# Kernel optimization log

Hardware: AMD Instinct MI355X
Metric: run time of the kernel (lower is better)

The kernel has to match this reference:

```python
import jax, jax.numpy as jnp
import numpy as np

B, N, D, H, C = 2048, 6, 2048, 1024, 200  # batch, nodes/graph, feat dim, hidden, classes
ALPHA = 0.015   # distance decay in edge weight
SCALE = 24.0    # weight rescale after mean-subtraction + clamp


def setup_inputs() -> dict:
    key = jax.random.key(0)
    k1, k2, k3, k4 = jax.random.split(key, 4)
    part_feats = jax.random.normal(k1, (B, N, D), dtype=jnp.float32)
    # cdds columns: [score, y0, x0, y1, x1, idx]; only cols 1:5 (box coords) are used
    cdds = jax.random.uniform(k2, (B, N, 6), dtype=jnp.float32) * 448.0
    fc_w = jax.random.normal(k3, (2 * D, H), dtype=jnp.float32) * 0.02
    fc_b = jnp.zeros((H,), dtype=jnp.float32)
    cls_w = jax.random.normal(k4, (H, C), dtype=jnp.float32) * 0.02
    cls_b = jnp.zeros((C,), dtype=jnp.float32)
    return {"part_feats": part_feats, "cdds": cdds, "fc_w": fc_w, "fc_b": fc_b,
            "cls_w": cls_w, "cls_b": cls_b}


def reference(part_feats, cdds, fc_w, fc_b, cls_w, cls_b):
    # --- edge weights on per-sample complete graph (apply_edges) ---
    loc = cdds[:, :, 1:5]                      # (B, N, 4) = (y0, x0, y1, x1)
    cy = (loc[..., 0] + loc[..., 2]) * 0.5     # node center y, (B, N)
    cx = (loc[..., 1] + loc[..., 3]) * 0.5     # node center x, (B, N)
    dx = cx[:, :, None] - cx[:, None, :]       # (B, N, N) pairwise
    dy = cy[:, :, None] - cy[:, None, :]
    d2 = dx * dx + dy * dy
    mask = ~jnp.eye(N, dtype=bool)             # off-diagonal = real edges (30 per graph)
    dist = jnp.sqrt(jnp.where(mask, d2, 1.0))  # safe sqrt off the diagonal
    w0 = jnp.where(mask, jnp.exp(-ALPHA * dist), 0.0)
    mean_w = jnp.sum(w0, axis=(1, 2), keepdims=True) / (N * (N - 1))  # mean over 30 edges
    w = SCALE * jnp.maximum(w0 - mean_w, 0.0) * mask                  # (B, N, N), w[b,u,v]
    # --- update_all: u_mul_e + mean over the (N-1) incoming edges per node ---
    hidden = jnp.einsum('buv,bud->bvd', w, part_feats) / (N - 1)      # (B, N, D)
    # --- node MLP + graph mean readout + classifier ---
    node_ft = jnp.concatenate([hidden, part_feats], axis=-1) @ fc_w + fc_b  # (B, N, H)
    g_ft = node_ft.mean(axis=1)                                             # (B, H)
    return g_ft @ cls_w + cls_b                                             # (B, C)
```

## Files before the change

kernel.cpp:

```cpp
#include <hip/hip_runtime.h>
#include <math.h>

namespace {
constexpr int NB = 2048;
constexpr int NNODE = 6;
constexpr int DD = 2048;
constexpr int HH = 1024;
constexpr int CC = 200;
constexpr int K2 = 2 * DD;
constexpr int NPAD = 256;
constexpr int ZF = 8;
constexpr float ALPHA_C = 0.015f;
constexpr float SCALE_C = 24.0f;
}

typedef __attribute__((ext_vector_type(8))) short bf16x8;
typedef __attribute__((ext_vector_type(4))) float f32x4;

static __device__ __forceinline__ unsigned short f2bf(float x) {
    union { float f; unsigned int u; } v; v.f = x;
    unsigned int r = v.u + 0x7FFFu + ((v.u >> 16) & 1u);
    return (unsigned short)(r >> 16);
}

static __device__ __forceinline__ float bf2f(unsigned short u) {
    union { unsigned int i; float f; } v; v.i = ((unsigned int)u) << 16;
    return v.f;
}

static __device__ __forceinline__ float compute_s_lane(const float* __restrict__ cdds,
                                                       int b, int* u_out) {
    const int lane = threadIdx.x & 63;
    const int u = lane >> 3;
    const int v = lane & 7;
    *u_out = u;
    const float* cd = cdds + (size_t)b * 36;
    float w = 0.f;
    const bool valid = (u < 6) & (v < 6) & (u != v);
    if (u < 6 && v < 6 && u != v) {
        float cyu = (cd[u * 6 + 1] + cd[u * 6 + 3]) * 0.5f;
        float cxu = (cd[u * 6 + 2] + cd[u * 6 + 4]) * 0.5f;
        float cyv = (cd[v * 6 + 1] + cd[v * 6 + 3]) * 0.5f;
        float cxv = (cd[v * 6 + 2] + cd[v * 6 + 4]) * 0.5f;
        float dx = cxu - cxv, dy = cyu - cyv;
        w = expf(-ALPHA_C * sqrtf(dx * dx + dy * dy));
    }
    float s = w;
#pragma unroll
    for (int m = 32; m >= 1; m >>= 1) s += __shfl_xor(s, m);
    float mean = s * (1.f / 30.f);
    float tt = valid ? fmaxf(w - mean, 0.f) : 0.f;
    tt += __shfl_xor(tt, 1);
    tt += __shfl_xor(tt, 2);
    tt += __shfl_xor(tt, 4);
    return SCALE_C * tt * 0.2f;
}

__global__ __launch_bounds__(256) void k_small(const float* __restrict__ cls_w,
                                               const float* __restrict__ fc_b,
                                               const float* __restrict__ cls_b,
                                               const float* __restrict__ cdds,
                                               float* __restrict__ bvec,
                                               float* __restrict__ sbuf)
{
    __shared__ float red[256];
    const int bx = blockIdx.x;
    const int t = threadIdx.x;
    if (bx >= 25) {
        const int b = (bx - 25) * 4 + (t >> 6);
        int u;
        float su = compute_s_lane(cdds, b, &u);
        if ((t & 7) == 0 && u < 6) sbuf[b * 6 + u] = su;
        return;
    }
    int c8 = t & 7;
    int hs = t >> 3;
    int c = bx * 8 + c8;
    float acc = 0.f;
    for (int h = hs; h < HH; h += 32)
        acc += fc_b[h] * cls_w[(size_t)h * CC + c];
    red[t] = acc;
    __syncthreads();
    for (int s = 128; s >= 8; s >>= 1) {
        if (t < s) red[t] += red[t + s];
        __syncthreads();
    }
    if (t < 8) bvec[c] = red[t] + cls_b[c];
}

__global__ __launch_bounds__(256) void k_g1(const float* __restrict__ fc_w,
                                            const float* __restrict__ cls_w,
                                            unsigned short* __restrict__ Mt)
{
    __shared__ short As[32][68];
    __shared__ short Bs[64][68];
    const int t = threadIdx.x;
    const int lane = t & 63;
    const int wid = t >> 6;
    const int wm = wid >> 1, wn = wid & 1;
    const int bm = blockIdx.x * 32;
    const int bn = blockIdx.y * 64;

    f32x4 acc[2] = {};

    for (int k0 = 0; k0 < HH; k0 += 64) {
#pragma unroll
        for (int c = 0; c < 2; ++c) {
            int i = t + c * 256;
            int row = i >> 4;
            int k4 = (i & 15) << 2;
            float4 v = *(const float4*)(fc_w + (size_t)(bm + row) * HH + k0 + k4);
            ushort4 o;
            o.x = f2bf(v.x); o.y = f2bf(v.y); o.z = f2bf(v.z); o.w = f2bf(v.w);
            *(ushort4*)&As[row][k4] = o;
        }
#pragma unroll
        for (int c = 0; c < 4; ++c) {
            int i = t + c * 256;
            int kr = i >> 4;
            int n4 = (i & 15) << 2;
            const float* sp = cls_w + (size_t)(k0 + kr) * CC + bn + n4;
            float4 v = {0.f, 0.f, 0.f, 0.f};
            if (bn + n4 + 3 < CC) {
                v = *(const float4*)sp;
            } else {
                if (bn + n4 + 0 < CC) v.x = sp[0];
                if (bn + n4 + 1 < CC) v.y = sp[1];
                if (bn + n4 + 2 < CC) v.z = sp[2];
                if (bn + n4 + 3 < CC) v.w = sp[3];
            }
            Bs[n4 + 0][kr] = (short)f2bf(v.x);
            Bs[n4 + 1][kr] = (short)f2bf(v.y);
            Bs[n4 + 2][kr] = (short)f2bf(v.z);
            Bs[n4 + 3][kr] = (short)f2bf(v.w);
        }
        __syncthreads();
#pragma unroll
        for (int ks = 0; ks < 2; ++ks) {
            int kk = ks * 32 + ((lane >> 4) << 3);
            int ar = lane & 15;
            bf16x8 a = *(const bf16x8*)&As[wm * 16 + ar][kk];
#pragma unroll
            for (int fn = 0; fn < 2; ++fn) {
                bf16x8 b = *(const bf16x8*)&Bs[wn * 32 + fn * 16 + ar][kk];
                acc[fn] = __builtin_amdgcn_mfma_f32_16x16x32_bf16(a, b, acc[fn], 0, 0, 0);
            }
        }
        __syncthreads();
    }
#pragma unroll
    for (int fn = 0; fn < 2; ++fn) {
        int gm0 = bm + wm * 16 + ((lane >> 4) << 2);
        int gn = bn + wn * 32 + fn * 16 + (lane & 15);
        ushort4 o;
        o.x = f2bf(acc[fn][0]); o.y = f2bf(acc[fn][1]);
        o.z = f2bf(acc[fn][2]); o.w = f2bf(acc[fn][3]);
        *(ushort4*)(Mt + (size_t)gn * K2 + gm0) = o;
    }
}

__global__ __launch_bounds__(256) void k_fused(const float* __restrict__ pf,
                                               const float* __restrict__ sbuf,
                                               const unsigned short* __restrict__ Mt,
                                               unsigned short* __restrict__ part)
{
    __shared__ short Ap[32][36], Aq[32][36];
    __shared__ short Bp[256][36], Bq[256][36];
    const int t = threadIdx.x;
    const int lane = t & 63;
    const int wid = t >> 6;
    const int bm = blockIdx.x * 32;
    const int z = blockIdx.y;
    const int kbase = z * (DD / ZF);

    const int r = t >> 3;
    const int k4 = (t & 7) << 2;
    const float* sb = sbuf + (size_t)(bm + r) * 6;
    const float s0 = sb[0], s1 = sb[1], s2 = sb[2];
    const float s3 = sb[3], s4 = sb[4], s5 = sb[5];
    const float* pfb = pf + (size_t)(bm + r) * NNODE * DD + kbase + k4;

    f32x4 acc[2][4] = {};

    for (int ks = 0; ks < (DD / ZF) / 32; ++ks) {
        const int k0 = ks * 32;
        float4 v0 = *(const float4*)(pfb + k0 + 0 * DD);
        float4 v1 = *(const float4*)(pfb + k0 + 1 * DD);
        float4 v2 = *(const float4*)(pfb + k0 + 2 * DD);
        float4 v3 = *(const float4*)(pfb + k0 + 3 * DD);
        float4 v4 = *(const float4*)(pfb + k0 + 4 * DD);
        float4 v5 = *(const float4*)(pfb + k0 + 5 * DD);
#pragma unroll
        for (int c = 0; c < 4; ++c) {
            int i = t + c * 256;
            int n = i >> 2;
            int k8 = (i & 3) << 3;
            *(uint4*)&Bp[n][k8] =
                *(const uint4*)(Mt + (size_t)n * K2 + kbase + k0 + k8);
            *(uint4*)&Bq[n][k8] =
                *(const uint4*)(Mt + (size_t)n * K2 + DD + kbase + k0 + k8);
        }
        float4 q;
        q.x = v0.x + v1.x + v2.x + v3.x + v4.x + v5.x;
        q.y = v0.y + v1.y + v2.y + v3.y + v4.y + v5.y;
        q.z = v0.z + v1.z + v2.z + v3.z + v4.z + v5.z;
        q.w = v0.w + v1.w + v2.w + v3.w + v4.w + v5.w;
        float4 p = {0.f, 0.f, 0.f, 0.f};
        p.x = fmaf(s0, v0.x, p.x); p.y = fmaf(s0, v0.y, p.y);
        p.z = fmaf(s0, v0.z, p.z); p.w = fmaf(s0, v0.w, p.w);
        p.x = fmaf(s1, v1.x, p.x); p.y = fmaf(s1, v1.y, p.y);
        p.z = fmaf(s1, v1.z, p.z); p.w = fmaf(s1, v1.w, p.w);
        p.x = fmaf(s2, v2.x, p.x); p.y = fmaf(s2, v2.y, p.y);
        p.z = fmaf(s2, v2.z, p.z); p.w = fmaf(s2, v2.w, p.w);
        p.x = fmaf(s3, v3.x, p.x); p.y = fmaf(s3, v3.y, p.y);
        p.z = fmaf(s3, v3.z, p.z); p.w = fmaf(s3, v3.w, p.w);
        p.x = fmaf(s4, v4.x, p.x); p.y = fmaf(s4, v4.y, p.y);
        p.z = fmaf(s4, v4.z, p.z); p.w = fmaf(s4, v4.w, p.w);
        p.x = fmaf(s5, v5.x, p.x); p.y = fmaf(s5, v5.y, p.y);
        p.z = fmaf(s5, v5.z, p.z); p.w = fmaf(s5, v5.w, p.w);
        ushort4 pb, qb;
        pb.x = f2bf(p.x); pb.y = f2bf(p.y); pb.z = f2bf(p.z); pb.w = f2bf(p.w);
        qb.x = f2bf(q.x); qb.y = f2bf(q.y); qb.z = f2bf(q.z); qb.w = f2bf(q.w);
        *(ushort4*)&Ap[r][k4] = pb;
        *(ushort4*)&Aq[r][k4] = qb;
        __syncthreads();
        {
            int kk = (lane >> 4) << 3;
            int ar = lane & 15;
            bf16x8 ap0 = *(const bf16x8*)&Ap[ar][kk];
            bf16x8 ap1 = *(const bf16x8*)&Ap[16 + ar][kk];
            bf16x8 aq0 = *(const bf16x8*)&Aq[ar][kk];
            bf16x8 aq1 = *(const bf16x8*)&Aq[16 + ar][kk];
#pragma unroll
            for (int fn = 0; fn < 4; ++fn) {
                bf16x8 bp = *(const bf16x8*)&Bp[wid * 64 + fn * 16 + ar][kk];
                bf16x8 bq = *(const bf16x8*)&Bq[wid * 64 + fn * 16 + ar][kk];
                acc[0][fn] = __builtin_amdgcn_mfma_f32_16x16x32_bf16(ap0, bp, acc[0][fn], 0, 0, 0);
                acc[1][fn] = __builtin_amdgcn_mfma_f32_16x16x32_bf16(ap1, bp, acc[1][fn], 0, 0, 0);
                acc[0][fn] = __builtin_amdgcn_mfma_f32_16x16x32_bf16(aq0, bq, acc[0][fn], 0, 0, 0);
                acc[1][fn] = __builtin_amdgcn_mfma_f32_16x16x32_bf16(aq1, bq, acc[1][fn], 0, 0, 0);
            }
        }
        __syncthreads();
    }
#pragma unroll
    for (int fm = 0; fm < 2; ++fm)
#pragma unroll
        for (int fn = 0; fn < 4; ++fn) {
            int gm0 = bm + fm * 16 + ((lane >> 4) << 2);
            int gn = wid * 64 + fn * 16 + (lane & 15);
#pragma unroll
            for (int rr = 0; rr < 4; ++rr)
                part[((size_t)z * NB + gm0 + rr) * NPAD + gn] = f2bf(acc[fm][fn][rr]);
        }
}

__global__ __launch_bounds__(256) void k_combine(const unsigned short* __restrict__ part,
                                                 const float* __restrict__ bvec,
                                                 float* __restrict__ out)
{
    int idx = blockIdx.x * blockDim.x + threadIdx.x;
    if (idx >= NB * (CC / 4)) return;
    int b = idx / (CC / 4);
    int c0 = (idx - b * (CC / 4)) << 2;
    float s0 = 0.f, s1 = 0.f, s2 = 0.f, s3 = 0.f;
#pragma unroll
    for (int z = 0; z < ZF; ++z) {
        ushort4 v = *(const ushort4*)(part + ((size_t)z * NB + b) * NPAD + c0);
        s0 += bf2f(v.x); s1 += bf2f(v.y); s2 += bf2f(v.z); s3 += bf2f(v.w);
    }
    float4 o;
    o.x = s0 * (1.f / 6.f) + bvec[c0 + 0];
    o.y = s1 * (1.f / 6.f) + bvec[c0 + 1];
    o.z = s2 * (1.f / 6.f) + bvec[c0 + 2];
    o.w = s3 * (1.f / 6.f) + bvec[c0 + 3];
    *(float4*)(out + (size_t)b * CC + c0) = o;
}

extern "C" void kernel_launch(void* const* d_in, const int* in_sizes, int n_in,
                              void* d_out, int out_size, void* d_ws, size_t ws_size,
                              hipStream_t stream)
{
    const float* part_feats = (const float*)d_in[0];
    const float* cdds = (const float*)d_in[1];
    const float* fc_w = (const float*)d_in[2];
    const float* fc_b = (const float*)d_in[3];
    const float* cls_w = (const float*)d_in[4];
    const float* cls_b = (const float*)d_in[5];
    float* out = (float*)d_out;

    char* ws = (char*)d_ws;
    size_t off = 0;
    unsigned short* Mt = (unsigned short*)(ws + off);   off += (size_t)NPAD * K2 * 2;
    unsigned short* part = (unsigned short*)(ws + off); off += (size_t)ZF * NB * NPAD * 2;
    float* bvec = (float*)(ws + off);                   off += 256 * 4;
    float* sbuf = (float*)(ws + off);                   off += (size_t)NB * NNODE * 4;

    k_small<<<dim3(25 + NB / 4), dim3(256), 0, stream>>>(
        cls_w, fc_b, cls_b, cdds, bvec, sbuf);
    k_g1<<<dim3(K2 / 32, NPAD / 64), dim3(256), 0, stream>>>(fc_w, cls_w, Mt);
    k_fused<<<dim3(NB / 32, ZF), dim3(256), 0, stream>>>(part_feats, sbuf, Mt, part);
    k_combine<<<dim3((NB * (CC / 4) + 255) / 256), dim3(256), 0, stream>>>(part, bvec, out);
}
```

Measured before the change: 86.23 us.

## Split node reduction into a bf16 pq buffer and run a plain split-K GEMM

The weighted and plain node reductions (p and q) move out of the GEMM kernel. They now run in extra blocks of the Mt-building kernel, which write a bf16 [B, 2D] activation buffer. The second GEMM becomes a standard bf16 GEMM with 64-row tiles, 64-deep K steps and 16-way split-K, reading that buffer. This lets the streaming pass over part_feats overlap with the small weight GEMM and gives the main GEMM more reuse per tile. In exchange it adds a round trip of the bf16 buffer through global memory and doubles the partial-sum traffic in the combine step.

```diff
diff --git a/kernel.cpp b/kernel.cpp
--- a/kernel.cpp
+++ b/kernel.cpp
@@ -9,9 +9,12 @@
 constexpr int CC = 200;
 constexpr int K2 = 2 * DD;
 constexpr int NPAD = 256;
-constexpr int ZF = 8;
+constexpr int ZS2 = 16;
 constexpr float ALPHA_C = 0.015f;
 constexpr float SCALE_C = 24.0f;
+
+constexpr int G1_BLOCKS = 512;
+constexpr int PQ_UNITS = NB * 2;
 }
 
 typedef __attribute__((ext_vector_type(8))) short bf16x8;
@@ -88,18 +91,70 @@
     if (t < 8) bvec[c] = red[t] + cls_b[c];
 }
 
-__global__ __launch_bounds__(256) void k_g1(const float* __restrict__ fc_w,
-                                            const float* __restrict__ cls_w,
-                                            unsigned short* __restrict__ Mt)
+__global__ __launch_bounds__(256) void k_mid(const float* __restrict__ pf,
+                                             const float* __restrict__ sbuf,
+                                             const float* __restrict__ fc_w,
+                                             const float* __restrict__ cls_w,
+                                             unsigned short* __restrict__ pq,
+                                             unsigned short* __restrict__ Mt)
 {
     __shared__ short As[32][68];
     __shared__ short Bs[64][68];
+    const int bx = blockIdx.x;
     const int t = threadIdx.x;
+
+    if (bx >= G1_BLOCKS) {
+        const int bid = bx - G1_BLOCKS;
+        const int virt = (bid & 7) * (PQ_UNITS / 8) + (bid >> 3);
+        const int b = virt >> 1;
+        const int d = ((virt & 1) << 10) + (t << 2);
+
+        const float* base = pf + (size_t)b * NNODE * DD + d;
+        float4 v0 = *(const float4*)(base + 0 * DD);
+        float4 v1 = *(const float4*)(base + 1 * DD);
+        float4 v2 = *(const float4*)(base + 2 * DD);
+        float4 v3 = *(const float4*)(base + 3 * DD);
+        float4 v4 = *(const float4*)(base + 4 * DD);
+        float4 v5 = *(const float4*)(base + 5 * DD);
+
+        const float* sb = sbuf + (size_t)b * 6;
+        float s0 = sb[0], s1 = sb[1], s2 = sb[2];
+        float s3 = sb[3], s4 = sb[4], s5 = sb[5];
+
+        float4 q;
+        q.x = v0.x + v1.x + v2.x + v3.x + v4.x + v5.x;
+        q.y = v0.y + v1.y + v2.y + v3.y + v4.y + v5.y;
+        q.z = v0.z + v1.z + v2.z + v3.z + v4.z + v5.z;
+        q.w = v0.w + v1.w + v2.w + v3.w + v4.w + v5.w;
+
+        float4 p = {0.f, 0.f, 0.f, 0.f};
+        p.x = fmaf(s0, v0.x, p.x); p.y = fmaf(s0, v0.y, p.y);
+        p.z = fmaf(s0, v0.z, p.z); p.w = fmaf(s0, v0.w, p.w);
+        p.x = fmaf(s1, v1.x, p.x); p.y = fmaf(s1, v1.y, p.y);
+        p.z = fmaf(s1, v1.z, p.z); p.w = fmaf(s1, v1.w, p.w);
+        p.x = fmaf(s2, v2.x, p.x); p.y = fmaf(s2, v2.y, p.y);
+        p.z = fmaf(s2, v2.z, p.z); p.w = fmaf(s2, v2.w, p.w);
+        p.x = fmaf(s3, v3.x, p.x); p.y = fmaf(s3, v3.y, p.y);
+        p.z = fmaf(s3, v3.z, p.z); p.w = fmaf(s3, v3.w, p.w);
+        p.x = fmaf(s4, v4.x, p.x); p.y = fmaf(s4, v4.y, p.y);
+        p.z = fmaf(s4, v4.z, p.z); p.w = fmaf(s4, v4.w, p.w);
+        p.x = fmaf(s5, v5.x, p.x); p.y = fmaf(s5, v5.y, p.y);
+        p.z = fmaf(s5, v5.z, p.z); p.w = fmaf(s5, v5.w, p.w);
+
+        unsigned short* o = pq + (size_t)b * K2;
+        ushort4 pb, qb;
+        pb.x = f2bf(p.x); pb.y = f2bf(p.y); pb.z = f2bf(p.z); pb.w = f2bf(p.w);
+        qb.x = f2bf(q.x); qb.y = f2bf(q.y); qb.z = f2bf(q.z); qb.w = f2bf(q.w);
+        *(ushort4*)(o + d) = pb;
+        *(ushort4*)(o + DD + d) = qb;
+        return;
+    }
+
     const int lane = t & 63;
     const int wid = t >> 6;
     const int wm = wid >> 1, wn = wid & 1;
-    const int bm = blockIdx.x * 32;
-    const int bn = blockIdx.y * 64;
+    const int bm = (bx >> 2) * 32;
+    const int bn = (bx & 3) * 64;
 
     f32x4 acc[2] = {};
 
@@ -159,99 +214,67 @@
     }
 }
 
-__global__ __launch_bounds__(256) void k_fused(const float* __restrict__ pf,
-                                               const float* __restrict__ sbuf,
-                                               const unsigned short* __restrict__ Mt,
+__global__ __launch_bounds__(256) void k_gemm2(const unsigned short* __restrict__ A,
+                                               const unsigned short* __restrict__ Bt,
                                                unsigned short* __restrict__ part)
 {
-    __shared__ short Ap[32][36], Aq[32][36];
-    __shared__ short Bp[256][36], Bq[256][36];
+    __shared__ short As[64][72];
+    __shared__ short Bs[256][72];
     const int t = threadIdx.x;
     const int lane = t & 63;
     const int wid = t >> 6;
-    const int bm = blockIdx.x * 32;
+    const int bm = blockIdx.x * 64;
     const int z = blockIdx.y;
-    const int kbase = z * (DD / ZF);
-
-    const int r = t >> 3;
-    const int k4 = (t & 7) << 2;
-    const float* sb = sbuf + (size_t)(bm + r) * 6;
-    const float s0 = sb[0], s1 = sb[1], s2 = sb[2];
-    const float s3 = sb[3], s4 = sb[4], s5 = sb[5];
-    const float* pfb = pf + (size_t)(bm + r) * NNODE * DD + kbase + k4;
-
-    f32x4 acc[2][4] = {};
-
-    for (int ks = 0; ks < (DD / ZF) / 32; ++ks) {
-        const int k0 = ks * 32;
-        float4 v0 = *(const float4*)(pfb + k0 + 0 * DD);
-        float4 v1 = *(const float4*)(pfb + k0 + 1 * DD);
-        float4 v2 = *(const float4*)(pfb + k0 + 2 * DD);
-        float4 v3 = *(const float4*)(pfb + k0 + 3 * DD);
-        float4 v4 = *(const float4*)(pfb + k0 + 4 * DD);
-        float4 v5 = *(const float4*)(pfb + k0 + 5 * DD);
-#pragma unroll
-        for (int c = 0; c < 4; ++c) {
+    const int kbase = z * (K2 / ZS2);
+
+    f32x4 acc[4][4] = {};
+
+    for (int k0 = kbase; k0 < kbase + K2 / ZS2; k0 += 64) {
+#pragma unroll
+        for (int c = 0; c < 2; ++c) {
             int i = t + c * 256;
-            int n = i >> 2;
-            int k8 = (i & 3) << 3;
-            *(uint4*)&Bp[n][k8] =
-                *(const uint4*)(Mt + (size_t)n * K2 + kbase + k0 + k8);
-            *(uint4*)&Bq[n][k8] =
-                *(const uint4*)(Mt + (size_t)n * K2 + DD + kbase + k0 + k8);
-        }
-        float4 q;
-        q.x = v0.x + v1.x + v2.x + v3.x + v4.x + v5.x;
-        q.y = v0.y + v1.y + v2.y + v3.y + v4.y + v5.y;
-        q.z = v0.z + v1.z + v2.z + v3.z + v4.z + v5.z;
-        q.w = v0.w + v1.w + v2.w + v3.w + v4.w + v5.w;
-        float4 p = {0.f, 0.f, 0.f, 0.f};
-        p.x = fmaf(s0, v0.x, p.x); p.y = fmaf(s0, v0.y, p.y);
-        p.z = fmaf(s0, v0.z, p.z); p.w = fmaf(s0, v0.w, p.w);
-        p.x = fmaf(s1, v1.x, p.x); p.y = fmaf(s1, v1.y, p.y);
-        p.z = fmaf(s1, v1.z, p.z); p.w = fmaf(s1, v1.w, p.w);
-        p.x = fmaf(s2, v2.x, p.x); p.y = fmaf(s2, v2.y, p.y);
-        p.z = fmaf(s2, v2.z, p.z); p.w = fmaf(s2, v2.w, p.w);
-        p.x = fmaf(s3, v3.x, p.x); p.y = fmaf(s3, v3.y, p.y);
-        p.z = fmaf(s3, v3.z, p.z); p.w = fmaf(s3, v3.w, p.w);
-        p.x = fmaf(s4, v4.x, p.x); p.y = fmaf(s4, v4.y, p.y);
-        p.z = fmaf(s4, v4.z, p.z); p.w = fmaf(s4, v4.w, p.w);
-        p.x = fmaf(s5, v5.x, p.x); p.y = fmaf(s5, v5.y, p.y);
-        p.z = fmaf(s5, v5.z, p.z); p.w = fmaf(s5, v5.w, p.w);
-        ushort4 pb, qb;
-        pb.x = f2bf(p.x); pb.y = f2bf(p.y); pb.z = f2bf(p.z); pb.w = f2bf(p.w);
-        qb.x = f2bf(q.x); qb.y = f2bf(q.y); qb.z = f2bf(q.z); qb.w = f2bf(q.w);
-        *(ushort4*)&Ap[r][k4] = pb;
-        *(ushort4*)&Aq[r][k4] = qb;
-        __syncthreads();
-        {
-            int kk = (lane >> 4) << 3;
+            int row = i >> 3;
+            int k8 = (i & 7) << 3;
+            *(uint4*)&As[row][k8] =
+                *(const uint4*)(A + (size_t)(bm + row) * K2 + k0 + k8);
+        }
+#pragma unroll
+        for (int c = 0; c < 8; ++c) {
+            int i = t + c * 256;
+            int n = i >> 3;
+            int k8 = (i & 7) << 3;
+            *(uint4*)&Bs[n][k8] =
+                *(const uint4*)(Bt + (size_t)n * K2 + k0 + k8);
+        }
+        __syncthreads();
+#pragma unroll
+        for (int ks = 0; ks < 2; ++ks) {
+            int kk = ks * 32 + ((lane >> 4) << 3);
             int ar = lane & 15;
-            bf16x8 ap0 = *(const bf16x8*)&Ap[ar][kk];
-            bf16x8 ap1 = *(const bf16x8*)&Ap[16 + ar][kk];
-            bf16x8 aq0 = *(const bf16x8*)&Aq[ar][kk];
-            bf16x8 aq1 = *(const bf16x8*)&Aq[16 + ar][kk];
+            bf16x8 a0 = *(const bf16x8*)&As[0 * 16 + ar][kk];
+            bf16x8 a1 = *(const bf16x8*)&As[1 * 16 + ar][kk];
+            bf16x8 a2 = *(const bf16x8*)&As[2 * 16 + ar][kk];
+            bf16x8 a3 = *(const bf16x8*)&As[3 * 16 + ar][kk];
 #pragma unroll
             for (int fn = 0; fn < 4; ++fn) {
-                bf16x8 bp = *(const bf16x8*)&Bp[wid * 64 + fn * 16 + ar][kk];
-                bf16x8 bq = *(const bf16x8*)&Bq[wid * 64 + fn * 16 + ar][kk];
-                acc[0][fn] = __builtin_amdgcn_mfma_f32_16x16x32_bf16(ap0, bp, acc[0][fn], 0, 0, 0);
-                acc[1][fn] = __builtin_amdgcn_mfma_f32_16x16x32_bf16(ap1, bp, acc[1][fn], 0, 0, 0);
-                acc[0][fn] = __builtin_amdgcn_mfma_f32_16x16x32_bf16(aq0, bq, acc[0][fn], 0, 0, 0);
-                acc[1][fn] = __builtin_amdgcn_mfma_f32_16x16x32_bf16(aq1, bq, acc[1][fn], 0, 0, 0);
+                bf16x8 b = *(const bf16x8*)&Bs[wid * 64 + fn * 16 + ar][kk];
+                acc[0][fn] = __builtin_amdgcn_mfma_f32_16x16x32_bf16(a0, b, acc[0][fn], 0, 0, 0);
+                acc[1][fn] = __builtin_amdgcn_mfma_f32_16x16x32_bf16(a1, b, acc[1][fn], 0, 0, 0);
+                acc[2][fn] = __builtin_amdgcn_mfma_f32_16x16x32_bf16(a2, b, acc[2][fn], 0, 0, 0);
+                acc[3][fn] = __builtin_amdgcn_mfma_f32_16x16x32_bf16(a3, b, acc[3][fn], 0, 0, 0);
             }
         }
         __syncthreads();
     }
 #pragma unroll
-    for (int fm = 0; fm < 2; ++fm)
+    for (int fm = 0; fm < 4; ++fm)
 #pragma unroll
         for (int fn = 0; fn < 4; ++fn) {
             int gm0 = bm + fm * 16 + ((lane >> 4) << 2);
             int gn = wid * 64 + fn * 16 + (lane & 15);
 #pragma unroll
-            for (int rr = 0; rr < 4; ++rr)
-                part[((size_t)z * NB + gm0 + rr) * NPAD + gn] = f2bf(acc[fm][fn][rr]);
+            for (int r = 0; r < 4; ++r)
+                part[((size_t)z * NB + gm0 + r) * NPAD + gn] = f2bf(acc[fm][fn][r]);
         }
 }
 
@@ -265,7 +288,7 @@
     int c0 = (idx - b * (CC / 4)) << 2;
     float s0 = 0.f, s1 = 0.f, s2 = 0.f, s3 = 0.f;
 #pragma unroll
-    for (int z = 0; z < ZF; ++z) {
+    for (int z = 0; z < ZS2; ++z) {
         ushort4 v = *(const ushort4*)(part + ((size_t)z * NB + b) * NPAD + c0);
         s0 += bf2f(v.x); s1 += bf2f(v.y); s2 += bf2f(v.z); s3 += bf2f(v.w);
     }
@@ -291,14 +314,16 @@
 
     char* ws = (char*)d_ws;
     size_t off = 0;
+    unsigned short* pq = (unsigned short*)(ws + off);   off += (size_t)NB * K2 * 2;
     unsigned short* Mt = (unsigned short*)(ws + off);   off += (size_t)NPAD * K2 * 2;
-    unsigned short* part = (unsigned short*)(ws + off); off += (size_t)ZF * NB * NPAD * 2;
+    unsigned short* part = (unsigned short*)(ws + off); off += (size_t)ZS2 * NB * NPAD * 2;
     float* bvec = (float*)(ws + off);                   off += 256 * 4;
     float* sbuf = (float*)(ws + off);                   off += (size_t)NB * NNODE * 4;
 
     k_small<<<dim3(25 + NB / 4), dim3(256), 0, stream>>>(
         cls_w, fc_b, cls_b, cdds, bvec, sbuf);
-    k_g1<<<dim3(K2 / 32, NPAD / 64), dim3(256), 0, stream>>>(fc_w, cls_w, Mt);
-    k_fused<<<dim3(NB / 32, ZF), dim3(256), 0, stream>>>(part_feats, sbuf, Mt, part);
+    k_mid<<<dim3(G1_BLOCKS + PQ_UNITS), dim3(256), 0, stream>>>(
+        part_feats, sbuf, fc_w, cls_w, pq, Mt);
+    k_gemm2<<<dim3(NB / 64, ZS2), dim3(256), 0, stream>>>(pq, Mt, part);
     k_combine<<<dim3((NB * (CC / 4) + 255) / 256), dim3(256), 0, stream>>>(part, bvec, out);
 }
```

After: 85.78 us. About the same (-0.5%).
